# Performance work log

Hardware: AMD Instinct MI355X
Metric: run time of the kernel (lower is better)

Reference implementation:

```python
import jax, jax.numpy as jnp
import numpy as np

N_NODES = 30000
E_EDGES = 480000
IN_DIM = 256
REL_DIM = 128
OUT_DIM = 512


def setup_inputs() -> dict:
    key = jax.random.key(0)
    ks = jax.random.split(key, 12)
    h = jax.random.normal(ks[0], (N_NODES, IN_DIM), dtype=jnp.float32)
    node_att = jax.random.uniform(ks[1], (N_NODES, 1), dtype=jnp.float32)
    rel = jax.random.normal(ks[2], (E_EDGES, REL_DIM), dtype=jnp.float32)
    edge_att = jax.random.uniform(ks[3], (E_EDGES, 1), dtype=jnp.float32)
    src = jax.random.randint(ks[4], (E_EDGES,), 0, N_NODES, dtype=jnp.int32)
    dst = jax.random.randint(ks[5], (E_EDGES,), 0, N_NODES, dtype=jnp.int32)
    # learned params (Linear: y = x @ W + b), scaled like default torch init
    def lin(k, fan_in, fan_out):
        k1, k2 = jax.random.split(k)
        bound = 1.0 / np.sqrt(fan_in)
        W = jax.random.uniform(k1, (fan_in, fan_out), minval=-bound, maxval=bound, dtype=jnp.float32)
        b = jax.random.uniform(k2, (fan_out,), minval=-bound, maxval=bound, dtype=jnp.float32)
        return W, b
    Wn, bn = lin(ks[6], IN_DIM, IN_DIM)
    Wr, br = lin(ks[7], REL_DIM, REL_DIM)
    Wa, ba = lin(ks[8], 2 * IN_DIM + REL_DIM, OUT_DIM)
    return {"h": h, "node_att": node_att, "rel": rel, "edge_att": edge_att,
            "Wn": Wn, "bn": bn, "Wr": Wr, "br": br, "Wa": Wa, "ba": ba,
            "src": src, "dst": dst}


def reference(h, node_att, rel, edge_att, Wn, bn, Wr, br, Wa, ba, src, dst):
    n_nodes = h.shape[0]
    # apply_nodes: h <- node_fc(h)  (runs BEFORE message passing)
    h2 = h @ Wn + bn                                   # [N, in]
    # message: z1 = att_src*h_src + att_dst*h_dst      [E, in]
    z1 = node_att[src] * h2[src] + node_att[dst] * h2[dst]
    # z2 = edge_att * rel_fc(rel)                      [E, rel]
    z2 = edge_att * (rel @ Wr + br)
    msg = jnp.concatenate([z1, z2], axis=1)            # [E, in+rel]
    # reduce: sum messages into destination nodes
    h_sum = jax.ops.segment_sum(msg, dst, num_segments=n_nodes)  # [N, in+rel]
    # apply_fc + relu on cat([h, h_sum])               [N, 2*in+rel] -> [N, out]
    out = jax.nn.relu(jnp.concatenate([h2, h_sum], axis=1) @ Wa + ba)
    return out
```

## Files before the change

### kernel.cpp

```cpp
#include <hip/hip_runtime.h>

#define E_EDGES 480000
#define N_NODES 30000
#define IN_DIM 256
#define REL_DIM 128
#define OUT_DIM 512
#define CAT_DIM 640
#define MTILES 1875

typedef float f32x4 __attribute__((ext_vector_type(4)));
typedef __bf16 bf16x8 __attribute__((ext_vector_type(8)));
typedef unsigned short u16x8 __attribute__((ext_vector_type(8)));

static __device__ __forceinline__ unsigned short f2bf(float x) {
    union { float f; unsigned int u; } c; c.f = x;
    unsigned int u = c.u;
    unsigned int r = u + 0x7fffu + ((u >> 16) & 1u);
    return (unsigned short)(r >> 16);
}
static __device__ __forceinline__ float bf2f(unsigned short b) {
    union { unsigned int u; float f; } c; c.u = ((unsigned int)b) << 16;
    return c.f;
}

__global__ void k_count(const int* __restrict__ dst, int* __restrict__ cnt) {
    int e = blockIdx.x * 256 + threadIdx.x;
    if (e < E_EDGES) atomicAdd(&cnt[dst[e]], 1);
}

__global__ void k_scan(const int* __restrict__ cnt, int* __restrict__ off,
                       int* __restrict__ cur) {
    __shared__ int part[1024];
    const int t = threadIdx.x;
    const int CH = (N_NODES + 1023) / 1024;
    int b = t * CH;
    int e = b + CH; if (e > N_NODES) e = N_NODES;
    if (b > N_NODES) b = N_NODES;
    int s = 0;
    for (int i = b; i < e; ++i) s += cnt[i];
    part[t] = s;
    __syncthreads();
    for (int d = 1; d < 1024; d <<= 1) {
        int v = (t >= d) ? part[t - d] : 0;
        __syncthreads();
        part[t] += v;
        __syncthreads();
    }
    int run = part[t] - s;
    for (int i = b; i < e; ++i) { off[i] = run; cur[i] = run; run += cnt[i]; }
    if (t == 1023) off[N_NODES] = run;
}

__global__ void k_fill(const int* __restrict__ dst, const int* __restrict__ src,
                       const float* __restrict__ eatt, const float* __restrict__ natt,
                       int* __restrict__ cur, int4* __restrict__ ecp) {
    int e = blockIdx.x * 256 + threadIdx.x;
    if (e < E_EDGES) {
        const int d = dst[e];
        const int s = src[e];
        const int p = atomicAdd(&cur[d], 1);
        ecp[p] = make_int4(e, s, __float_as_int(eatt[e]), __float_as_int(natt[s]));
    }
}

template <int K, int NCOLS>
__launch_bounds__(512)
__global__ void gemm_As(const float* __restrict__ Ag,
                        const float* __restrict__ Bg,
                        const float* __restrict__ bias,
                        const float* __restrict__ rowb,
                        unsigned short* __restrict__ Cg,
                        int ldc, int mtiles) {
    constexpr int KB = K / 32;
    constexpr int LDB = K + 8;
    __shared__ unsigned short Bt[64 * LDB];
    unsigned int* Bt32 = (unsigned int*)Bt;

    const int lane = threadIdx.x & 63;
    const int wave = threadIdx.x >> 6;
    const int row16 = lane & 15;
    const int kgrp = lane >> 4;
    const int mt = blockIdx.x * 8 + wave;
    const bool active = (mt < mtiles);

    bf16x8 af[KB];
    {
        const float* arow = Ag + (size_t)((active ? mt : 0) * 16 + row16) * K + kgrp * 8;
#pragma unroll
        for (int kb = 0; kb < KB; ++kb) {
            f32x4 x0 = *(const f32x4*)(arow + kb * 32);
            f32x4 x1 = *(const f32x4*)(arow + kb * 32 + 4);
            u16x8 au;
#pragma unroll
            for (int j = 0; j < 4; ++j) { au[j] = f2bf(x0[j]); au[4 + j] = f2bf(x1[j]); }
            af[kb] = __builtin_bit_cast(bf16x8, au);
        }
    }

    for (int nc0 = 0; nc0 < NCOLS; nc0 += 64) {
        __syncthreads();
        for (int idx = threadIdx.x; idx < 64 * (K / 2); idx += 512) {
            const int n = idx & 63;
            const int kp = idx >> 6;
            const float x0 = Bg[(size_t)(2 * kp) * NCOLS + nc0 + n];
            const float x1 = Bg[(size_t)(2 * kp + 1) * NCOLS + nc0 + n];
            Bt32[n * (LDB / 2) + kp] = (unsigned int)f2bf(x0) | ((unsigned int)f2bf(x1) << 16);
        }
        __syncthreads();
        if (active) {
            f32x4 acc[4] = {};
#pragma unroll
            for (int kb = 0; kb < KB; ++kb) {
#pragma unroll
                for (int nt = 0; nt < 4; ++nt) {
                    bf16x8 bf = *(const bf16x8*)(&Bt[(nt * 16 + row16) * LDB + kb * 32 + kgrp * 8]);
                    acc[nt] = __builtin_amdgcn_mfma_f32_16x16x32_bf16(af[kb], bf, acc[nt], 0, 0, 0);
                }
            }
#pragma unroll
            for (int nt = 0; nt < 4; ++nt) {
                const int ocol = nc0 + nt * 16 + row16;
                const float bv = bias[ocol];
#pragma unroll
                for (int r = 0; r < 4; ++r) {
                    const int orow = mt * 16 + kgrp * 4 + r;
                    float v = acc[nt][r] + (rowb ? rowb[orow] * bv : bv);
                    Cg[(size_t)orow * ldc + ocol] = f2bf(v);
                }
            }
        }
    }
}

__launch_bounds__(128)
__global__ void k_gather(unsigned short* __restrict__ Amat,
                         const float* __restrict__ rel,
                         const float* __restrict__ natt,
                         const int* __restrict__ off,
                         const int4* __restrict__ ecp,
                         float* __restrict__ R,
                         float* __restrict__ S) {
    const int n = blockIdx.x;
    const int t = threadIdx.x;
    const int b = off[n], e = off[n + 1];
    float a0 = 0.f, a1 = 0.f, ar = 0.f, ae = 0.f;
    int i = b;
    for (; i + 2 <= e; i += 2) {
        const int4 p0 = ecp[i];
        const int4 p1 = ecp[i + 1];
        const unsigned int hv0 = *(const unsigned int*)(Amat + (size_t)p0.y * CAT_DIM + 2 * t);
        const float r0 = rel[(size_t)p0.x * REL_DIM + t];
        const unsigned int hv1 = *(const unsigned int*)(Amat + (size_t)p1.y * CAT_DIM + 2 * t);
        const float r1 = rel[(size_t)p1.x * REL_DIM + t];
        const float ea0 = __int_as_float(p0.z), w0 = __int_as_float(p0.w);
        const float ea1 = __int_as_float(p1.z), w1 = __int_as_float(p1.w);
        a0 += w0 * bf2f((unsigned short)(hv0 & 0xffffu)) + w1 * bf2f((unsigned short)(hv1 & 0xffffu));
        a1 += w0 * bf2f((unsigned short)(hv0 >> 16)) + w1 * bf2f((unsigned short)(hv1 >> 16));
        ar += ea0 * r0 + ea1 * r1;
        ae += ea0 + ea1;
    }
    if (i < e) {
        const int4 p0 = ecp[i];
        const unsigned int hv0 = *(const unsigned int*)(Amat + (size_t)p0.y * CAT_DIM + 2 * t);
        const float r0 = rel[(size_t)p0.x * REL_DIM + t];
        const float ea0 = __int_as_float(p0.z), w0 = __int_as_float(p0.w);
        a0 += w0 * bf2f((unsigned short)(hv0 & 0xffffu));
        a1 += w0 * bf2f((unsigned short)(hv0 >> 16));
        ar += ea0 * r0;
        ae += ea0;
    }
    const int deg = e - b;
    if (deg > 0) {
        const float w = (float)deg * natt[n];
        const unsigned int hv = *(const unsigned int*)(Amat + (size_t)n * CAT_DIM + 2 * t);
        a0 += w * bf2f((unsigned short)(hv & 0xffffu));
        a1 += w * bf2f((unsigned short)(hv >> 16));
    }
    const unsigned int packed = (unsigned int)f2bf(a0) | ((unsigned int)f2bf(a1) << 16);
    *(unsigned int*)(Amat + (size_t)n * CAT_DIM + IN_DIM + 2 * t) = packed;
    R[(size_t)n * REL_DIM + t] = ar;
    if (t == 0) S[n] = ae;
}

__launch_bounds__(512)
__global__ void gemm_final(const unsigned short* __restrict__ Ag,
                           const float* __restrict__ Wa,
                           const float* __restrict__ ba,
                           float* __restrict__ out) {
    constexpr int KCH = 64;
    constexpr int LDB = KCH + 8;
    __shared__ unsigned short Bt[256 * LDB];
    unsigned int* Bt32 = (unsigned int*)Bt;
    const int nc0 = blockIdx.y * 256;

    const int lane = threadIdx.x & 63;
    const int wave = threadIdx.x >> 6;
    const int row16 = lane & 15;
    const int kgrp = lane >> 4;
    const int mt0 = blockIdx.x * 16 + wave * 2;
    const int mt1 = mt0 + 1;
    const bool act0 = (mt0 < MTILES);
    const bool act1 = (mt1 < MTILES);

    f32x4 acc0[16] = {};
    f32x4 acc1[16] = {};
    const unsigned short* arow0 =
        Ag + (size_t)((act0 ? mt0 : 0) * 16 + row16) * CAT_DIM + kgrp * 8;
    const unsigned short* arow1 =
        Ag + (size_t)((act1 ? mt1 : 0) * 16 + row16) * CAT_DIM + kgrp * 8;

    for (int kc = 0; kc < CAT_DIM / KCH; ++kc) {
        __syncthreads();
        for (int idx = threadIdx.x; idx < 256 * (KCH / 2); idx += 512) {
            const int n = idx & 255;
            const int kp = idx >> 8;
            const int k = kc * KCH + 2 * kp;
            const float x0 = Wa[(size_t)k * OUT_DIM + nc0 + n];
            const float x1 = Wa[(size_t)(k + 1) * OUT_DIM + nc0 + n];
            Bt32[n * (LDB / 2) + kp] = (unsigned int)f2bf(x0) | ((unsigned int)f2bf(x1) << 16);
        }
        __syncthreads();
#pragma unroll
        for (int kb = 0; kb < 2; ++kb) {
            bf16x8 a0 = __builtin_bit_cast(bf16x8, *(const u16x8*)(arow0 + kc * KCH + kb * 32));
            bf16x8 a1 = __builtin_bit_cast(bf16x8, *(const u16x8*)(arow1 + kc * KCH + kb * 32));
#pragma unroll
            for (int nt = 0; nt < 16; ++nt) {
                bf16x8 bf = *(const bf16x8*)(&Bt[(nt * 16 + row16) * LDB + kb * 32 + kgrp * 8]);
                acc0[nt] = __builtin_amdgcn_mfma_f32_16x16x32_bf16(a0, bf, acc0[nt], 0, 0, 0);
                acc1[nt] = __builtin_amdgcn_mfma_f32_16x16x32_bf16(a1, bf, acc1[nt], 0, 0, 0);
            }
        }
    }
    if (act0) {
#pragma unroll
        for (int nt = 0; nt < 16; ++nt) {
            const int ocol = nc0 + nt * 16 + row16;
            const float bv = ba[ocol];
#pragma unroll
            for (int r = 0; r < 4; ++r) {
                const int orow = mt0 * 16 + kgrp * 4 + r;
                out[(size_t)orow * OUT_DIM + ocol] = fmaxf(acc0[nt][r] + bv, 0.0f);
            }
        }
    }
    if (act1) {
#pragma unroll
        for (int nt = 0; nt < 16; ++nt) {
            const int ocol = nc0 + nt * 16 + row16;
            const float bv = ba[ocol];
#pragma unroll
            for (int r = 0; r < 4; ++r) {
                const int orow = mt1 * 16 + kgrp * 4 + r;
                out[(size_t)orow * OUT_DIM + ocol] = fmaxf(acc1[nt][r] + bv, 0.0f);
            }
        }
    }
}

extern "C" void kernel_launch(void* const* d_in, const int* in_sizes, int n_in,
                              void* d_out, int out_size, void* d_ws, size_t ws_size,
                              hipStream_t stream) {
    const float* h    = (const float*)d_in[0];
    const float* natt = (const float*)d_in[1];
    const float* rel  = (const float*)d_in[2];
    const float* eatt = (const float*)d_in[3];
    const float* Wn   = (const float*)d_in[4];
    const float* bn   = (const float*)d_in[5];
    const float* Wr   = (const float*)d_in[6];
    const float* br   = (const float*)d_in[7];
    const float* Wa   = (const float*)d_in[8];
    const float* ba   = (const float*)d_in[9];
    const int* src    = (const int*)d_in[10];
    const int* dst    = (const int*)d_in[11];
    float* out = (float*)d_out;

    char* base = (char*)d_ws;
    unsigned short* Amat = (unsigned short*)(base);
    float* R = (float*)(base + 38400000);
    float* S = (float*)(base + 53760000);
    int* cnt = (int*)(base + 53880064);
    int* off = (int*)(base + 54000064);
    int* cur = (int*)(base + 54120128);
    int4* ecp = (int4*)(base + 54240128);

    hipMemsetAsync(cnt, 0, N_NODES * sizeof(int), stream);
    k_count<<<(E_EDGES + 255) / 256, 256, 0, stream>>>(dst, cnt);
    k_scan<<<1, 1024, 0, stream>>>(cnt, off, cur);
    k_fill<<<(E_EDGES + 255) / 256, 256, 0, stream>>>(dst, src, eatt, natt, cur, ecp);

    gemm_As<256, 256><<<235, 512, 0, stream>>>(h, Wn, bn, nullptr, Amat, CAT_DIM, MTILES);

    k_gather<<<N_NODES, 128, 0, stream>>>(Amat, rel, natt, off, ecp, R, S);

    gemm_As<128, 128><<<235, 512, 0, stream>>>(R, Wr, br, S, Amat + 2 * IN_DIM, CAT_DIM, MTILES);

    gemm_final<<<dim3(118, 2), 512, 0, stream>>>(Amat, Wa, ba, out);
}
```

Before: 613.3 us.

## Pre-pack weights into MFMA-ready bf16 layout and read B fragments directly

Adds a prep kernel that converts Wn, Wr and Wa to bf16 once, in a layout where each lane's MFMA B fragment is a contiguous 16-byte load. The GEMMs then drop the per-block LDS transpose/convert staging and its syncthreads, and fetch B straight from global/L2. This removes the redundant fp32 weight conversion that every block repeated. In exchange, each wave issues more global loads and the fully unrolled gemm_final raises register pressure. The gather loop is also unrolled to 4 edges per iteration to keep more loads in flight.

```diff
diff --git a/kernel.cpp b/kernel.cpp
--- a/kernel.cpp
+++ b/kernel.cpp
@@ -63,19 +63,36 @@
     }
 }
 
-template <int K, int NCOLS>
+__global__ void k_prep(const float* __restrict__ Wn, const float* __restrict__ Wr,
+                       const float* __restrict__ Wa,
+                       unsigned short* __restrict__ WnT,
+                       unsigned short* __restrict__ WrT,
+                       unsigned short* __restrict__ WaT) {
+    const int fid = blockIdx.x * 256 + threadIdx.x;
+    const float* Bg; unsigned short* WT; int N; int idx;
+    if (fid < 8192)        { Bg = Wn; WT = WnT; N = 256; idx = fid; }
+    else if (fid < 10240)  { Bg = Wr; WT = WrT; N = 128; idx = fid - 8192; }
+    else if (fid < 51200)  { Bg = Wa; WT = WaT; N = 512; idx = fid - 10240; }
+    else return;
+    const int c = idx % N;
+    const int t = idx / N;
+    const int k0 = t * 8;
+    u16x8 v;
+#pragma unroll
+    for (int j = 0; j < 8; ++j) v[j] = f2bf(Bg[(size_t)(k0 + j) * N + c]);
+    *(u16x8*)(WT + (size_t)idx * 8) = v;
+}
+
+template <int K, int N>
 __launch_bounds__(512)
-__global__ void gemm_As(const float* __restrict__ Ag,
-                        const float* __restrict__ Bg,
-                        const float* __restrict__ bias,
-                        const float* __restrict__ rowb,
-                        unsigned short* __restrict__ Cg,
-                        int ldc, int mtiles) {
+__global__ void gemm_reg(const float* __restrict__ Ag,
+                         const unsigned short* __restrict__ Btab,
+                         const float* __restrict__ bias,
+                         const float* __restrict__ rowb,
+                         unsigned short* __restrict__ Cg,
+                         int ldc, int mtiles) {
     constexpr int KB = K / 32;
-    constexpr int LDB = K + 8;
-    __shared__ unsigned short Bt[64 * LDB];
-    unsigned int* Bt32 = (unsigned int*)Bt;
-
+    constexpr int NT = N / 16;
     const int lane = threadIdx.x & 63;
     const int wave = threadIdx.x >> 6;
     const int row16 = lane & 15;
@@ -97,36 +114,27 @@
         }
     }
 
-    for (int nc0 = 0; nc0 < NCOLS; nc0 += 64) {
-        __syncthreads();
-        for (int idx = threadIdx.x; idx < 64 * (K / 2); idx += 512) {
-            const int n = idx & 63;
-            const int kp = idx >> 6;
-            const float x0 = Bg[(size_t)(2 * kp) * NCOLS + nc0 + n];
-            const float x1 = Bg[(size_t)(2 * kp + 1) * NCOLS + nc0 + n];
-            Bt32[n * (LDB / 2) + kp] = (unsigned int)f2bf(x0) | ((unsigned int)f2bf(x1) << 16);
-        }
-        __syncthreads();
-        if (active) {
-            f32x4 acc[4] = {};
-#pragma unroll
-            for (int kb = 0; kb < KB; ++kb) {
-#pragma unroll
-                for (int nt = 0; nt < 4; ++nt) {
-                    bf16x8 bf = *(const bf16x8*)(&Bt[(nt * 16 + row16) * LDB + kb * 32 + kgrp * 8]);
-                    acc[nt] = __builtin_amdgcn_mfma_f32_16x16x32_bf16(af[kb], bf, acc[nt], 0, 0, 0);
-                }
-            }
-#pragma unroll
-            for (int nt = 0; nt < 4; ++nt) {
-                const int ocol = nc0 + nt * 16 + row16;
-                const float bv = bias[ocol];
-#pragma unroll
-                for (int r = 0; r < 4; ++r) {
-                    const int orow = mt * 16 + kgrp * 4 + r;
-                    float v = acc[nt][r] + (rowb ? rowb[orow] * bv : bv);
-                    Cg[(size_t)orow * ldc + ocol] = f2bf(v);
-                }
+    const unsigned short* pB = Btab + (size_t)(kgrp * N + row16) * 8;
+    f32x4 acc[NT] = {};
+#pragma unroll
+    for (int kb = 0; kb < KB; ++kb) {
+        const unsigned short* pBk = pB + (size_t)kb * 4 * N * 8;
+#pragma unroll
+        for (int nt = 0; nt < NT; ++nt) {
+            bf16x8 bf = *(const bf16x8*)(pBk + nt * 128);
+            acc[nt] = __builtin_amdgcn_mfma_f32_16x16x32_bf16(af[kb], bf, acc[nt], 0, 0, 0);
+        }
+    }
+    if (active) {
+#pragma unroll
+        for (int nt = 0; nt < NT; ++nt) {
+            const int ocol = nt * 16 + row16;
+            const float bv = bias[ocol];
+#pragma unroll
+            for (int r = 0; r < 4; ++r) {
+                const int orow = mt * 16 + kgrp * 4 + r;
+                float v = acc[nt][r] + (rowb ? rowb[orow] * bv : bv);
+                Cg[(size_t)orow * ldc + ocol] = f2bf(v);
             }
         }
     }
@@ -145,21 +153,31 @@
     const int b = off[n], e = off[n + 1];
     float a0 = 0.f, a1 = 0.f, ar = 0.f, ae = 0.f;
     int i = b;
-    for (; i + 2 <= e; i += 2) {
+    for (; i + 4 <= e; i += 4) {
         const int4 p0 = ecp[i];
         const int4 p1 = ecp[i + 1];
+        const int4 p2 = ecp[i + 2];
+        const int4 p3 = ecp[i + 3];
         const unsigned int hv0 = *(const unsigned int*)(Amat + (size_t)p0.y * CAT_DIM + 2 * t);
+        const unsigned int hv1 = *(const unsigned int*)(Amat + (size_t)p1.y * CAT_DIM + 2 * t);
+        const unsigned int hv2 = *(const unsigned int*)(Amat + (size_t)p2.y * CAT_DIM + 2 * t);
+        const unsigned int hv3 = *(const unsigned int*)(Amat + (size_t)p3.y * CAT_DIM + 2 * t);
         const float r0 = rel[(size_t)p0.x * REL_DIM + t];
-        const unsigned int hv1 = *(const unsigned int*)(Amat + (size_t)p1.y * CAT_DIM + 2 * t);
         const float r1 = rel[(size_t)p1.x * REL_DIM + t];
+        const float r2 = rel[(size_t)p2.x * REL_DIM + t];
+        const float r3 = rel[(size_t)p3.x * REL_DIM + t];
         const float ea0 = __int_as_float(p0.z), w0 = __int_as_float(p0.w);
         const float ea1 = __int_as_float(p1.z), w1 = __int_as_float(p1.w);
-        a0 += w0 * bf2f((unsigned short)(hv0 & 0xffffu)) + w1 * bf2f((unsigned short)(hv1 & 0xffffu));
-        a1 += w0 * bf2f((unsigned short)(hv0 >> 16)) + w1 * bf2f((unsigned short)(hv1 >> 16));
-        ar += ea0 * r0 + ea1 * r1;
-        ae += ea0 + ea1;
-    }
-    if (i < e) {
+        const float ea2 = __int_as_float(p2.z), w2 = __int_as_float(p2.w);
+        const float ea3 = __int_as_float(p3.z), w3 = __int_as_float(p3.w);
+        a0 += w0 * bf2f((unsigned short)(hv0 & 0xffffu)) + w1 * bf2f((unsigned short)(hv1 & 0xffffu))
+            + w2 * bf2f((unsigned short)(hv2 & 0xffffu)) + w3 * bf2f((unsigned short)(hv3 & 0xffffu));
+        a1 += w0 * bf2f((unsigned short)(hv0 >> 16)) + w1 * bf2f((unsigned short)(hv1 >> 16))
+            + w2 * bf2f((unsigned short)(hv2 >> 16)) + w3 * bf2f((unsigned short)(hv3 >> 16));
+        ar += ea0 * r0 + ea1 * r1 + ea2 * r2 + ea3 * r3;
+        ae += ea0 + ea1 + ea2 + ea3;
+    }
+    for (; i < e; ++i) {
         const int4 p0 = ecp[i];
         const unsigned int hv0 = *(const unsigned int*)(Amat + (size_t)p0.y * CAT_DIM + 2 * t);
         const float r0 = rel[(size_t)p0.x * REL_DIM + t];
@@ -184,19 +202,14 @@
 
 __launch_bounds__(512)
 __global__ void gemm_final(const unsigned short* __restrict__ Ag,
-                           const float* __restrict__ Wa,
+                           const unsigned short* __restrict__ WaT,
                            const float* __restrict__ ba,
                            float* __restrict__ out) {
-    constexpr int KCH = 64;
-    constexpr int LDB = KCH + 8;
-    __shared__ unsigned short Bt[256 * LDB];
-    unsigned int* Bt32 = (unsigned int*)Bt;
-    const int nc0 = blockIdx.y * 256;
-
     const int lane = threadIdx.x & 63;
     const int wave = threadIdx.x >> 6;
     const int row16 = lane & 15;
     const int kgrp = lane >> 4;
+    const int nc0 = blockIdx.y * 256;
     const int mt0 = blockIdx.x * 16 + wave * 2;
     const int mt1 = mt0 + 1;
     const bool act0 = (mt0 < MTILES);
@@ -208,28 +221,18 @@
         Ag + (size_t)((act0 ? mt0 : 0) * 16 + row16) * CAT_DIM + kgrp * 8;
     const unsigned short* arow1 =
         Ag + (size_t)((act1 ? mt1 : 0) * 16 + row16) * CAT_DIM + kgrp * 8;
-
-    for (int kc = 0; kc < CAT_DIM / KCH; ++kc) {
-        __syncthreads();
-        for (int idx = threadIdx.x; idx < 256 * (KCH / 2); idx += 512) {
-            const int n = idx & 255;
-            const int kp = idx >> 8;
-            const int k = kc * KCH + 2 * kp;
-            const float x0 = Wa[(size_t)k * OUT_DIM + nc0 + n];
-            const float x1 = Wa[(size_t)(k + 1) * OUT_DIM + nc0 + n];
-            Bt32[n * (LDB / 2) + kp] = (unsigned int)f2bf(x0) | ((unsigned int)f2bf(x1) << 16);
-        }
-        __syncthreads();
-#pragma unroll
-        for (int kb = 0; kb < 2; ++kb) {
-            bf16x8 a0 = __builtin_bit_cast(bf16x8, *(const u16x8*)(arow0 + kc * KCH + kb * 32));
-            bf16x8 a1 = __builtin_bit_cast(bf16x8, *(const u16x8*)(arow1 + kc * KCH + kb * 32));
-#pragma unroll
-            for (int nt = 0; nt < 16; ++nt) {
-                bf16x8 bf = *(const bf16x8*)(&Bt[(nt * 16 + row16) * LDB + kb * 32 + kgrp * 8]);
-                acc0[nt] = __builtin_amdgcn_mfma_f32_16x16x32_bf16(a0, bf, acc0[nt], 0, 0, 0);
-                acc1[nt] = __builtin_amdgcn_mfma_f32_16x16x32_bf16(a1, bf, acc1[nt], 0, 0, 0);
-            }
+    const unsigned short* pB = WaT + (size_t)(kgrp * OUT_DIM + nc0 + row16) * 8;
+
+#pragma unroll
+    for (int kb = 0; kb < CAT_DIM / 32; ++kb) {
+        bf16x8 a0 = __builtin_bit_cast(bf16x8, *(const u16x8*)(arow0 + kb * 32));
+        bf16x8 a1 = __builtin_bit_cast(bf16x8, *(const u16x8*)(arow1 + kb * 32));
+        const unsigned short* pBk = pB + (size_t)kb * 4 * OUT_DIM * 8;
+#pragma unroll
+        for (int nt = 0; nt < 16; ++nt) {
+            bf16x8 bf = *(const bf16x8*)(pBk + nt * 128);
+            acc0[nt] = __builtin_amdgcn_mfma_f32_16x16x32_bf16(a0, bf, acc0[nt], 0, 0, 0);
+            acc1[nt] = __builtin_amdgcn_mfma_f32_16x16x32_bf16(a1, bf, acc1[nt], 0, 0, 0);
         }
     }
     if (act0) {
@@ -283,17 +286,21 @@
     int* off = (int*)(base + 54000064);
     int* cur = (int*)(base + 54120128);
     int4* ecp = (int4*)(base + 54240128);
+    unsigned short* WnT = (unsigned short*)(base + 61920128);
+    unsigned short* WrT = (unsigned short*)(base + 62051200);
+    unsigned short* WaT = (unsigned short*)(base + 62083968);
 
     hipMemsetAsync(cnt, 0, N_NODES * sizeof(int), stream);
     k_count<<<(E_EDGES + 255) / 256, 256, 0, stream>>>(dst, cnt);
     k_scan<<<1, 1024, 0, stream>>>(cnt, off, cur);
     k_fill<<<(E_EDGES + 255) / 256, 256, 0, stream>>>(dst, src, eatt, natt, cur, ecp);
-
-    gemm_As<256, 256><<<235, 512, 0, stream>>>(h, Wn, bn, nullptr, Amat, CAT_DIM, MTILES);
+    k_prep<<<200, 256, 0, stream>>>(Wn, Wr, Wa, WnT, WrT, WaT);
+
+    gemm_reg<256, 256><<<235, 512, 0, stream>>>(h, WnT, bn, nullptr, Amat, CAT_DIM, MTILES);
 
     k_gather<<<N_NODES, 128, 0, stream>>>(Amat, rel, natt, off, ecp, R, S);
 
-    gemm_As<128, 128><<<235, 512, 0, stream>>>(R, Wr, br, S, Amat + 2 * IN_DIM, CAT_DIM, MTILES);
-
-    gemm_final<<<dim3(118, 2), 512, 0, stream>>>(Amat, Wa, ba, out);
-}
+    gemm_reg<128, 128><<<235, 512, 0, stream>>>(R, WrT, br, S, Amat + 2 * IN_DIM, CAT_DIM, MTILES);
+
+    gemm_final<<<dim3(118, 2), 512, 0, stream>>>(Amat, WaT, ba, out);
+}
```

Measured after the change: 617.1 us. Within noise of the previous version (+0.6%).
